# Optimization experiments

Measured on AMD Instinct MI355X. Metric: run time of the kernel, lower is better.

The kernel has to match this reference:

```python
import jax, jax.numpy as jnp
import numpy as np


def _ln(x, g, b, eps=1e-5):
    m = jnp.mean(x, axis=-1, keepdims=True)
    v = jnp.mean((x - m) ** 2, axis=-1, keepdims=True)
    return (x - m) * jax.lax.rsqrt(v + eps) * g + b


def _mlp2(x, w1, b1, w2, b2):
    # Linear -> SiLU -> Linear
    return jax.nn.silu(x @ w1 + b1) @ w2 + b2


def setup_inputs() -> dict:
    key = jax.random.key(0)
    ks = jax.random.split(key, 32)
    B, H, W = 1, 128, 256
    N = H * W                  # 32768 nodes
    K = 6
    E = N * K                  # 196608 edges
    Cin, Cout = 70, 69
    D, De, Hd, L = 256, 128, 512, 8
    s = 0.02

    def rn(k, shape):
        return jax.random.normal(k, shape, jnp.float32) * s

    inp = {
        "x": jax.random.normal(ks[0], (B, Cin, H, W), jnp.float32),
        "edge_index": jax.random.randint(ks[1], (2, E), 0, N, dtype=jnp.int32).astype(jnp.int64),
        "raw_edge_feat": jax.random.normal(ks[2], (E, 3), jnp.float32),
        # node encoder
        "enc_w1": rn(ks[3], (Cin, D)), "enc_b1": jnp.zeros((D,), jnp.float32),
        "enc_w2": rn(ks[4], (D, D)),   "enc_b2": jnp.zeros((D,), jnp.float32),
        # edge encoder
        "eenc_w1": rn(ks[5], (3, De)),  "eenc_b1": jnp.zeros((De,), jnp.float32),
        "eenc_w2": rn(ks[6], (De, De)), "eenc_b2": jnp.zeros((De,), jnp.float32),
        # processor (stacked over L layers)
        "pe_w1": rn(ks[7], (L, 2 * D + De, Hd)), "pe_b1": jnp.zeros((L, Hd), jnp.float32),
        "pe_w2": rn(ks[8], (L, Hd, De)),         "pe_b2": jnp.zeros((L, De), jnp.float32),
        "pe_g": jnp.ones((L, De), jnp.float32),  "pe_bt": jnp.zeros((L, De), jnp.float32),
        "pn_w1": rn(ks[9], (L, D + De, Hd)),     "pn_b1": jnp.zeros((L, Hd), jnp.float32),
        "pn_w2": rn(ks[10], (L, Hd, D)),         "pn_b2": jnp.zeros((L, D), jnp.float32),
        "pn_g": jnp.ones((L, D), jnp.float32),   "pn_bt": jnp.zeros((L, D), jnp.float32),
        # node decoder
        "dec_w1": rn(ks[11], (D, D)),   "dec_b1": jnp.zeros((D,), jnp.float32),
        "dec_w2": rn(ks[12], (D, Cout)), "dec_b2": jnp.zeros((Cout,), jnp.float32),
    }
    return inp


def reference(x, edge_index, raw_edge_feat,
              enc_w1, enc_b1, enc_w2, enc_b2,
              eenc_w1, eenc_b1, eenc_w2, eenc_b2,
              pe_w1, pe_b1, pe_w2, pe_b2, pe_g, pe_bt,
              pn_w1, pn_b1, pn_w2, pn_b2, pn_g, pn_bt,
              dec_w1, dec_b1, dec_w2, dec_b2):
    B, C, H, W = x.shape
    N = H * W
    src, dst = edge_index[0], edge_index[1]

    # encode: (B, N, Cin) -> (B, N, D)
    node = _mlp2(jnp.transpose(x.reshape(B, C, N), (0, 2, 1)), enc_w1, enc_b1, enc_w2, enc_b2)
    # edge encoder shared across batch, then broadcast to (B, E, De)
    edge = _mlp2(raw_edge_feat, eenc_w1, eenc_b1, eenc_w2, eenc_b2)
    edge = jnp.broadcast_to(edge[None], (B,) + edge.shape)

    def step(carry, p):
        node, edge = carry
        ew1, eb1, ew2, eb2, eg, ebt, nw1, nb1, nw2, nb2, ng, nbt = p
        # edge update: gather src/dst node feats, residual MLP + LayerNorm
        inp = jnp.concatenate([node[:, src], node[:, dst], edge], axis=-1)  # (B, E, 2D+De)
        edge = _ln(edge + _mlp2(inp, ew1, eb1, ew2, eb2), eg, ebt)
        # aggregate edges into destination nodes (scatter_add)
        agg = jax.vmap(lambda e: jax.ops.segment_sum(e, dst, num_segments=N))(edge)
        # node update: residual MLP + LayerNorm
        node = _ln(node + _mlp2(jnp.concatenate([node, agg], axis=-1), nw1, nb1, nw2, nb2), ng, nbt)
        return (node, edge), None

    (node, edge), _ = jax.lax.scan(
        step, (node, edge),
        (pe_w1, pe_b1, pe_w2, pe_b2, pe_g, pe_bt,
         pn_w1, pn_b1, pn_w2, pn_b2, pn_g, pn_bt))

    out = _mlp2(node, dec_w1, dec_b1, dec_w2, dec_b2)          # (B, N, Cout)
    return jnp.transpose(out, (0, 2, 1)).reshape(B, -1, H, W)   # (B, Cout, H, W)
```

## Files before the change

### kernel.cpp

```cpp
#include <hip/hip_runtime.h>


typedef __attribute__((ext_vector_type(8))) short bf16x8;
typedef __attribute__((ext_vector_type(4))) float f32x4;
typedef unsigned short u16;

#define NNODES 32768
#define NEDGES 196608

#define MFMA16(a, b, c) __builtin_amdgcn_mfma_f32_16x16x32_bf16((a), (b), (c), 0, 0, 0)

__device__ __forceinline__ u16 f2bf(float f) {
    unsigned u = __float_as_uint(f);
    unsigned r = (u + 0x7FFFu + ((u >> 16) & 1u)) >> 16;
    return (u16)r;
}
__device__ __forceinline__ float bf2f(u16 b) {
    return __uint_as_float(((unsigned)b) << 16);
}
__device__ __forceinline__ unsigned pack2(float a, float b) {
    return (unsigned)f2bf(a) | ((unsigned)f2bf(b) << 16);
}

__global__ void wtrans_kernel(const float* __restrict__ W, u16* __restrict__ WT,
                              int K, int Nout, int Kpad, int NP) {
    __shared__ u16 tile[32][33];
    const int k0 = blockIdx.x * 32, n0 = blockIdx.y * 32;
    const int tx = threadIdx.x & 31, ty = threadIdx.x >> 5;
    #pragma unroll
    for (int i = 0; i < 4; i++) {
        int k = k0 + ty + 8 * i, n = n0 + tx;
        float v = (k < K && n < Nout) ? W[(size_t)k * Nout + n] : 0.f;
        tile[ty + 8 * i][tx] = f2bf(v);
    }
    __syncthreads();
    #pragma unroll
    for (int i = 0; i < 4; i++) {
        int n = n0 + ty + 8 * i, k = k0 + tx;
        if (n < NP && k < Kpad) WT[(size_t)n * Kpad + k] = tile[tx][ty + 8 * i];
    }
}

__global__ void fragpack_kernel(const float* __restrict__ W, u16* __restrict__ F,
                                int K, int N, int CB, int NFRAG) {
    int b = blockIdx.z;
    int fr = blockIdx.x * 4 + (threadIdx.x >> 6);
    if (fr >= NFRAG) return;
    int l = threadIdx.x & 63;
    int ks = fr / CB, cb = fr % CB;
    int k0 = ks * 32 + ((l >> 4) * 8);
    int n = cb * 16 + (l & 15);
    u16 v[8];
    #pragma unroll
    for (int j = 0; j < 8; j++) {
        int k = k0 + j;
        float x = (k < K && n < N) ? W[((size_t)b * K + k) * N + n] : 0.f;
        v[j] = f2bf(x);
    }
    *(uint4*)(F + (((size_t)b * NFRAG + fr) * 64 + l) * 8) = *(const uint4*)v;
}

__global__ void idx_norm_kernel(const int* __restrict__ raw, int* __restrict__ sd) {
    __shared__ int nz;
    if (threadIdx.x == 0) nz = 0;
    __syncthreads();
    for (int i = threadIdx.x; i < 512; i += 256)
        if (raw[2 * i + 1] != 0) atomicAdd(&nz, 1);
    __syncthreads();
    const bool is64 = (nz == 0);
    int idx = blockIdx.x * 256 + threadIdx.x;
    if (idx < 2 * NEDGES) sd[idx] = is64 ? raw[2 * idx] : raw[idx];
}

__global__ void csr_count_kernel(const int* __restrict__ dsti, int* __restrict__ deg) {
    int e = blockIdx.x * 256 + threadIdx.x;
    atomicAdd(&deg[dsti[e]], 1);
}

__global__ void csr_scan_kernel(const int* __restrict__ deg, int* __restrict__ off,
                                int* __restrict__ cur) {
    __shared__ int part[1024];
    const int t = threadIdx.x;
    int local[32];
    int s = 0;
    #pragma unroll
    for (int i = 0; i < 32; i++) { local[i] = deg[t * 32 + i]; s += local[i]; }
    part[t] = s;
    __syncthreads();
    for (int d = 1; d < 1024; d <<= 1) {
        int v = (t >= d) ? part[t - d] : 0;
        __syncthreads();
        part[t] += v;
        __syncthreads();
    }
    int excl = (t == 0) ? 0 : part[t - 1];
    #pragma unroll
    for (int i = 0; i < 32; i++) {
        off[t * 32 + i] = excl;
        cur[t * 32 + i] = excl;
        excl += local[i];
    }
    if (t == 1023) off[NNODES] = excl;
}

__global__ void csr_fill_kernel(const int* __restrict__ dsti, int* __restrict__ cur,
                                int* __restrict__ perm) {
    int e = blockIdx.x * 256 + threadIdx.x;
    int pos = atomicAdd(&cur[dsti[e]], 1);
    perm[pos] = e;
}

__global__ void esort_kernel(const int* __restrict__ sd, const int* __restrict__ perm,
                             int* __restrict__ srcS, int* __restrict__ dstS) {
    int i = blockIdx.x * 256 + threadIdx.x;
    int e = perm[i];
    srcS[i] = sd[e];
    dstS[i] = sd[NEDGES + e];
}

__global__ void gather_kernel(const u16* __restrict__ edge_b,
                              const int* __restrict__ off, u16* __restrict__ aggB) {
    int idx = blockIdx.x * 256 + threadIdx.x;
    int n = idx >> 5, c = (idx & 31) * 4;
    int a = off[n], b = off[n + 1];
    float s0 = 0.f, s1 = 0.f, s2 = 0.f, s3 = 0.f;
    for (int i = a; i < b; i++) {
        uint2 v = *(const uint2*)(edge_b + (size_t)i * 128 + c);
        s0 += bf2f((u16)(v.x & 0xffff)); s1 += bf2f((u16)(v.x >> 16));
        s2 += bf2f((u16)(v.y & 0xffff)); s3 += bf2f((u16)(v.y >> 16));
    }
    uint2 o;
    o.x = pack2(s0, s1);
    o.y = pack2(s2, s3);
    *(uint2*)(aggB + (size_t)n * 128 + c) = o;
}

struct MlpP {
    const u16* A1;
    const u16* A1b;
    const float* Araw;
    const int* src;
    const int* dsti;
    const u16* W1F;
    const u16* W2F;
    const float* b1;
    const float* b2;
    const float* g;
    const float* bt;
    const u16* residB;
    u16* outB;
    float* outDec;
};

template <int K1, int NH, int NOUT, int IN, int OUT, int A1S>
__global__ __launch_bounds__(256, 2) void mlp_kernel(MlpP p) {
    static_assert(K1 % 32 == 0 && NH % 128 == 0, "dims");
    constexpr int KSTEPS = K1 / 32;
    constexpr int NT1 = NH / 64;
    constexpr int CB1 = NH / 16;
    constexpr int NFRAG2 = (NOUT + 15) / 16;
    constexpr int NT2 = (NFRAG2 + 3) / 4;
    constexpr int S2 = NH / 64;
    constexpr int SH2 = NH / 2 + 8;
    constexpr int SH_BYTES = 64 * SH2 * 2;
    constexpr int SMEM_I = (SH_BYTES > 8192 ? SH_BYTES : 8192);
    constexpr int SMEM = SMEM_I + 2560;

    __shared__ __align__(16) char smem[SMEM];
    u16* sA = (u16*)smem;
    u16* sH = (u16*)smem;
    float* sS1 = (float*)(smem + SMEM_I);
    float* sS2 = sS1 + 256;
    float* sMu = sS1 + 512;
    float* sRs = sS1 + 576;

    const int tid = threadIdx.x;
    const int wave = tid >> 6, lane = tid & 63;
    const int lhi = lane >> 4, llo = lane & 15;
    const int r0 = blockIdx.x * 64;
    const int key = (llo >> 1) & 3;

    const int sr = tid >> 2;
    const int sg = (tid & 3) ^ ((sr >> 1) & 3);
    int gsrc = 0, gdst = 0;
    if constexpr (IN == 0) { gsrc = p.src[r0 + sr]; gdst = p.dsti[r0 + sr]; }
    if constexpr (IN == 3) { gsrc = p.src[r0 + sr]; }

    auto loadA = [&](int ks, uint4& d) {
        const int kb = ks * 32;
        if constexpr (IN == 0) {
            if (kb < 256)      d = *(const uint4*)(p.A1 + (size_t)gsrc * 256 + kb + sg * 8);
            else if (kb < 512) d = *(const uint4*)(p.A1 + (size_t)gdst * 256 + (kb - 256) + sg * 8);
            else               d = *(const uint4*)(p.A1b + (size_t)(r0 + sr) * 128 + (kb - 512) + sg * 8);
        } else if constexpr (IN == 1) {
            if (kb < 256) d = *(const uint4*)(p.A1 + (size_t)(r0 + sr) * 256 + kb + sg * 8);
            else          d = *(const uint4*)(p.A1b + (size_t)(r0 + sr) * 128 + (kb - 256) + sg * 8);
        } else if constexpr (IN == 2) {
            d = *(const uint4*)(p.A1 + (size_t)(r0 + sr) * A1S + kb + sg * 8);
        } else {
            uint4 v = {0u, 0u, 0u, 0u};
            if (sg == 0) {
                const float* q = p.Araw + (size_t)gsrc * 3;
                v.x = pack2(q[0], q[1]);
                v.y = pack2(q[2], 0.f);
            }
            d = v;
        }
    };
    auto loadB1 = [&](int ks, bf16x8 (&d)[NT1]) {
        #pragma unroll
        for (int j = 0; j < NT1; j++) {
            int cb = j * 4 + wave;
            d[j] = *(const bf16x8*)(p.W1F + ((size_t)(ks * CB1 + cb) * 64 + lane) * 8);
        }
    };

    const f32x4 fz = {0.f, 0.f, 0.f, 0.f};
    f32x4 acc[4][NT1];
    #pragma unroll
    for (int m = 0; m < 4; m++)
        #pragma unroll
        for (int j = 0; j < NT1; j++) acc[m][j] = fz;

    uint4 pa0, pa1, pa2;
    bf16x8 pb0[NT1], pb1[NT1];
    loadA(0, pa0);
    if constexpr (KSTEPS > 1) loadA(1, pa1);
    if constexpr (KSTEPS > 2) loadA(2, pa2);
    loadB1(0, pb0);
    if constexpr (KSTEPS > 1) loadB1(1, pb1);

    #pragma unroll
    for (int ks = 0; ks < KSTEPS; ks++) {
        uint4* sAw = (uint4*)(sA + (ks & 1) * 2048);
        sAw[tid] = (ks % 3 == 0) ? pa0 : (ks % 3 == 1) ? pa1 : pa2;
        if (ks + 3 < KSTEPS) {
            if (ks % 3 == 0) loadA(ks + 3, pa0);
            else if (ks % 3 == 1) loadA(ks + 3, pa1);
            else loadA(ks + 3, pa2);
        }
        __syncthreads();
        const u16* sAr = sA + (ks & 1) * 2048;
        bf16x8 a[4];
        #pragma unroll
        for (int m = 0; m < 4; m++)
            a[m] = *(const bf16x8*)(sAr + (m * 16 + llo) * 32 + (lhi ^ key) * 8);
        bf16x8 (&pbc)[NT1] = (ks & 1) ? pb1 : pb0;
        #pragma unroll
        for (int j = 0; j < NT1; j++)
            #pragma unroll
            for (int m = 0; m < 4; m++) acc[m][j] = MFMA16(a[m], pbc[j], acc[m][j]);
        if (ks + 2 < KSTEPS) loadB1(ks + 2, pbc);
    }
    __syncthreads();

    f32x4 acc2[4][NT2];
    #pragma unroll
    for (int m = 0; m < 4; m++)
        #pragma unroll
        for (int j = 0; j < NT2; j++) acc2[m][j] = fz;

    auto loadW2 = [&](int g, bf16x8 (&d)[NT2]) {
        #pragma unroll
        for (int j = 0; j < NT2; j++) {
            int f = j * 4 + wave;
            if (NFRAG2 % 4 == 0 || f < NFRAG2)
                d[j] = *(const bf16x8*)(p.W2F + ((size_t)(g * NFRAG2 + f) * 64 + lane) * 8);
        }
    };
    bf16x8 pw0[NT2], pw1[NT2];
    loadW2(0, pw0);
    loadW2(1, pw1);

    #pragma unroll
    for (int half = 0; half < 2; half++) {
        #pragma unroll
        for (int j = half * (NT1 / 2); j < (half + 1) * (NT1 / 2); j++) {
            int c = (j * 4 + wave) * 16 + llo;
            int coll = c - half * (NH / 2);
            float bias = p.b1[c];
            #pragma unroll
            for (int m = 0; m < 4; m++)
                #pragma unroll
                for (int r = 0; r < 4; r++) {
                    int row = m * 16 + lhi * 4 + r;
                    float v = acc[m][j][r] + bias;
                    float sgm = __builtin_amdgcn_rcpf(1.f + __expf(-v));
                    sH[row * SH2 + coll] = f2bf(v * sgm);
                }
        }
        __syncthreads();
        #pragma unroll
        for (int s = 0; s < S2; s++) {
            const int g = half * S2 + s;
            bf16x8 (&pwc)[NT2] = (g & 1) ? pw1 : pw0;
            bf16x8 a2[4];
            #pragma unroll
            for (int m = 0; m < 4; m++)
                a2[m] = *(const bf16x8*)(sH + (m * 16 + llo) * SH2 + s * 32 + lhi * 8);
            #pragma unroll
            for (int j = 0; j < NT2; j++)
                if (NFRAG2 % 4 == 0 || j * 4 + wave < NFRAG2)
                    #pragma unroll
                    for (int m = 0; m < 4; m++)
                        acc2[m][j] = MFMA16(a2[m], pwc[j], acc2[m][j]);
            if (g + 2 < 2 * S2) loadW2(g + 2, pwc);
        }
        __syncthreads();
    }

    if constexpr (OUT == 0) {
        float ps1[4][4], ps2[4][4];
        #pragma unroll
        for (int m = 0; m < 4; m++)
            #pragma unroll
            for (int r = 0; r < 4; r++) { ps1[m][r] = 0.f; ps2[m][r] = 0.f; }
        #pragma unroll
        for (int j = 0; j < NT2; j++) {
            int col = (j * 4 + wave) * 16 + llo;
            float bias = p.b2[col];
            #pragma unroll
            for (int m = 0; m < 4; m++)
                #pragma unroll
                for (int r = 0; r < 4; r++) {
                    int row = m * 16 + lhi * 4 + r;
                    float v = acc2[m][j][r] + bias +
                              bf2f(p.residB[(size_t)(r0 + row) * NOUT + col]);
                    acc2[m][j][r] = v;
                    ps1[m][r] += v;
                    ps2[m][r] += v * v;
                }
        }
        #pragma unroll
        for (int mm = 1; mm < 16; mm <<= 1)
            #pragma unroll
            for (int m = 0; m < 4; m++)
                #pragma unroll
                for (int r = 0; r < 4; r++) {
                    ps1[m][r] += __shfl_xor(ps1[m][r], mm, 64);
                    ps2[m][r] += __shfl_xor(ps2[m][r], mm, 64);
                }
        if (llo == 0) {
            #pragma unroll
            for (int m = 0; m < 4; m++)
                #pragma unroll
                for (int r = 0; r < 4; r++) {
                    int row = m * 16 + lhi * 4 + r;
                    sS1[wave * 64 + row] = ps1[m][r];
                    sS2[wave * 64 + row] = ps2[m][r];
                }
        }
        __syncthreads();
        if (tid < 64) {
            float a = sS1[tid] + sS1[64 + tid] + sS1[128 + tid] + sS1[192 + tid];
            float b = sS2[tid] + sS2[64 + tid] + sS2[128 + tid] + sS2[192 + tid];
            float mu = a * (1.f / NOUT);
            float var = b * (1.f / NOUT) - mu * mu;
            sMu[tid] = mu;
            sRs[tid] = rsqrtf(var + 1e-5f);
        }
        __syncthreads();
        #pragma unroll
        for (int j = 0; j < NT2; j++) {
            int col = (j * 4 + wave) * 16 + llo;
            float gg = p.g[col], bb = p.bt[col];
            #pragma unroll
            for (int m = 0; m < 4; m++)
                #pragma unroll
                for (int r = 0; r < 4; r++) {
                    int row = m * 16 + lhi * 4 + r;
                    float v = (acc2[m][j][r] - sMu[row]) * sRs[row] * gg + bb;
                    p.outB[(size_t)(r0 + row) * NOUT + col] = f2bf(v);
                }
        }
    } else if constexpr (OUT == 1) {
        #pragma unroll
        for (int j = 0; j < NT2; j++) {
            int col = (j * 4 + wave) * 16 + llo;
            float bias = p.b2[col];
            #pragma unroll
            for (int m = 0; m < 4; m++)
                #pragma unroll
                for (int r = 0; r < 4; r++) {
                    int row = m * 16 + lhi * 4 + r;
                    float v = acc2[m][j][r] + bias;
                    p.outB[(size_t)(r0 + row) * NOUT + col] = f2bf(v);
                }
        }
    } else {
        #pragma unroll
        for (int j = 0; j < NT2; j++) {
            int f = j * 4 + wave;
            int col = f * 16 + llo;
            if (f < NFRAG2 && col < 69) {
                float bias = p.b2[col];
                #pragma unroll
                for (int m = 0; m < 4; m++)
                    #pragma unroll
                    for (int r = 0; r < 4; r++) {
                        int row = m * 16 + lhi * 4 + r;
                        p.outDec[(size_t)col * NNODES + (r0 + row)] = acc2[m][j][r] + bias;
                    }
            }
        }
    }
}

extern "C" void kernel_launch(void* const* d_in, const int* in_sizes, int n_in,
                              void* d_out, int out_size, void* d_ws, size_t ws_size,
                              hipStream_t stream) {
    (void)in_sizes; (void)n_in; (void)out_size; (void)ws_size;

    const float* x       = (const float*)d_in[0];
    const int*   eidx    = (const int*)d_in[1];
    const float* raw_e   = (const float*)d_in[2];
    const float* enc_w1  = (const float*)d_in[3];
    const float* enc_b1  = (const float*)d_in[4];
    const float* enc_w2  = (const float*)d_in[5];
    const float* enc_b2  = (const float*)d_in[6];
    const float* eenc_w1 = (const float*)d_in[7];
    const float* eenc_b1 = (const float*)d_in[8];
    const float* eenc_w2 = (const float*)d_in[9];
    const float* eenc_b2 = (const float*)d_in[10];
    const float* pe_w1   = (const float*)d_in[11];
    const float* pe_b1   = (const float*)d_in[12];
    const float* pe_w2   = (const float*)d_in[13];
    const float* pe_b2   = (const float*)d_in[14];
    const float* pe_g    = (const float*)d_in[15];
    const float* pe_bt   = (const float*)d_in[16];
    const float* pn_w1   = (const float*)d_in[17];
    const float* pn_b1   = (const float*)d_in[18];
    const float* pn_w2   = (const float*)d_in[19];
    const float* pn_b2   = (const float*)d_in[20];
    const float* pn_g    = (const float*)d_in[21];
    const float* pn_bt   = (const float*)d_in[22];
    const float* dec_w1  = (const float*)d_in[23];
    const float* dec_b1  = (const float*)d_in[24];
    const float* dec_w2  = (const float*)d_in[25];
    const float* dec_b2  = (const float*)d_in[26];

    char* ws = (char*)d_ws;
    size_t o = 0;
    auto alloc = [&](size_t bytes) -> void* {
        void* p = ws + o;
        o += (bytes + 255) & ~(size_t)255;
        return p;
    };
    u16*   node_b = (u16*)  alloc((size_t)NNODES * 256 * 2);
    u16*   edge_b = (u16*)  alloc((size_t)NEDGES * 128 * 2);
    u16*   aggB   = (u16*)  alloc((size_t)NNODES * 128 * 2);
    u16*   xT     = (u16*)  alloc((size_t)NNODES * 96 * 2);
    u16*   encw1F  = (u16*)alloc((size_t)96 * 256 * 2);
    u16*   encw2F  = (u16*)alloc((size_t)256 * 256 * 2);
    u16*   eencw1F = (u16*)alloc((size_t)32 * 128 * 2);
    u16*   eencw2F = (u16*)alloc((size_t)128 * 128 * 2);
    u16*   pew1F   = (u16*)alloc((size_t)8 * 640 * 512 * 2);
    u16*   pew2F   = (u16*)alloc((size_t)8 * 512 * 128 * 2);
    u16*   pnw1F   = (u16*)alloc((size_t)8 * 384 * 512 * 2);
    u16*   pnw2F   = (u16*)alloc((size_t)8 * 512 * 256 * 2);
    u16*   decw1F  = (u16*)alloc((size_t)256 * 256 * 2);
    u16*   decw2F  = (u16*)alloc((size_t)256 * 80 * 2);
    int*   sd     = (int*)  alloc((size_t)2 * NEDGES * 4);
    int*   deg    = (int*)  alloc((size_t)NNODES * 4);
    int*   off_   = (int*)  alloc((size_t)(NNODES + 1) * 4);
    int*   cur    = (int*)  alloc((size_t)NNODES * 4);
    int*   perm   = (int*)  alloc((size_t)NEDGES * 4);
    int*   srcS   = (int*)  alloc((size_t)NEDGES * 4);
    int*   dstS   = (int*)  alloc((size_t)NEDGES * 4);

    auto FP = [&](const float* W, u16* F, int K, int N, int KB, int CB, int batch) {
        int nf = KB * CB;
        dim3 g((nf + 3) / 4, 1, batch);
        fragpack_kernel<<<g, 256, 0, stream>>>(W, F, K, N, CB, nf);
    };
    FP(enc_w1,  encw1F,  70,  256, 3,  16, 1);
    FP(enc_w2,  encw2F,  256, 256, 8,  16, 1);
    FP(eenc_w1, eencw1F, 3,   128, 1,  8,  1);
    FP(eenc_w2, eencw2F, 128, 128, 4,  8,  1);
    FP(pe_w1,   pew1F,   640, 512, 20, 32, 8);
    FP(pe_w2,   pew2F,   512, 128, 16, 8,  8);
    FP(pn_w1,   pnw1F,   384, 512, 12, 32, 8);
    FP(pn_w2,   pnw2F,   512, 256, 16, 16, 8);
    FP(dec_w1,  decw1F,  256, 256, 8,  16, 1);
    FP(dec_w2,  decw2F,  256, 69,  8,  5,  1);
    {
        dim3 g(96 / 32, NNODES / 32, 1);
        wtrans_kernel<<<g, 256, 0, stream>>>(x, xT, 70, NNODES, 96, NNODES);
    }

    idx_norm_kernel<<<1536, 256, 0, stream>>>(eidx, sd);
    hipMemsetAsync(deg, 0, (size_t)NNODES * 4, stream);
    csr_count_kernel<<<NEDGES / 256, 256, 0, stream>>>(sd + NEDGES, deg);
    csr_scan_kernel<<<1, 1024, 0, stream>>>(deg, off_, cur);
    csr_fill_kernel<<<NEDGES / 256, 256, 0, stream>>>(sd + NEDGES, cur, perm);
    esort_kernel<<<NEDGES / 256, 256, 0, stream>>>(sd, perm, srcS, dstS);

    {
        MlpP p{};
        p.A1 = xT; p.W1F = encw1F; p.W2F = encw2F; p.b1 = enc_b1; p.b2 = enc_b2;
        p.outB = node_b;
        mlp_kernel<96, 256, 256, 2, 1, 96><<<NNODES / 64, 256, 0, stream>>>(p);
    }
    {
        MlpP p{};
        p.Araw = raw_e; p.src = perm;
        p.W1F = eencw1F; p.W2F = eencw2F; p.b1 = eenc_b1; p.b2 = eenc_b2;
        p.outB = edge_b;
        mlp_kernel<32, 128, 128, 3, 1, 0><<<NEDGES / 64, 256, 0, stream>>>(p);
    }

    for (int l = 0; l < 8; l++) {
        {
            MlpP p{};
            p.A1 = node_b; p.A1b = edge_b; p.src = srcS; p.dsti = dstS;
            p.W1F = pew1F + (size_t)l * 640 * 512;
            p.W2F = pew2F + (size_t)l * 512 * 128;
            p.b1 = pe_b1 + l * 512; p.b2 = pe_b2 + l * 128;
            p.g = pe_g + l * 128; p.bt = pe_bt + l * 128;
            p.residB = edge_b; p.outB = edge_b;
            mlp_kernel<640, 512, 128, 0, 0, 0><<<NEDGES / 64, 256, 0, stream>>>(p);
        }
        gather_kernel<<<NNODES * 32 / 256, 256, 0, stream>>>(edge_b, off_, aggB);
        {
            MlpP p{};
            p.A1 = node_b; p.A1b = aggB;
            p.W1F = pnw1F + (size_t)l * 384 * 512;
            p.W2F = pnw2F + (size_t)l * 512 * 256;
            p.b1 = pn_b1 + l * 512; p.b2 = pn_b2 + l * 256;
            p.g = pn_g + l * 256; p.bt = pn_bt + l * 256;
            p.residB = node_b; p.outB = node_b;
            mlp_kernel<384, 512, 256, 1, 0, 0><<<NNODES / 64, 256, 0, stream>>>(p);
        }
    }

    {
        MlpP p{};
        p.A1 = node_b; p.W1F = decw1F; p.W2F = decw2F; p.b1 = dec_b1; p.b2 = dec_b2;
        p.outDec = (float*)d_out;
        mlp_kernel<256, 256, 80, 2, 2, 256><<<NNODES / 64, 256, 0, stream>>>(p);
    }
}
```

Baseline: 2.043 ms.

## Switch MLP kernel from 16x16x32 to 32x32x16 bf16 MFMA tiles

Replaces the 16x16x32 MFMA instructions in the fused two-layer MLP kernel with 32x32x16 MFMA, reorganizing accumulators into 32x32 blocks, the LDS A-fragment reads, the weight fragment packing layout, and all epilogue row/column mappings. Larger MFMA tiles give more output per instruction and fewer A/B fragment loads per flop. The cost is larger accumulator register footprint per wave and different LDS bank access patterns. Small-width layers like the encoder may end up with partially filled tiles.

```diff
diff --git a/kernel.cpp b/kernel.cpp
--- a/kernel.cpp
+++ b/kernel.cpp
@@ -2,13 +2,13 @@
 
 
 typedef __attribute__((ext_vector_type(8))) short bf16x8;
-typedef __attribute__((ext_vector_type(4))) float f32x4;
+typedef __attribute__((ext_vector_type(16))) float f32x16;
 typedef unsigned short u16;
 
 #define NNODES 32768
 #define NEDGES 196608
 
-#define MFMA16(a, b, c) __builtin_amdgcn_mfma_f32_16x16x32_bf16((a), (b), (c), 0, 0, 0)
+#define MFMA32(a, b, c) __builtin_amdgcn_mfma_f32_32x32x16_bf16((a), (b), (c), 0, 0, 0)
 
 __device__ __forceinline__ u16 f2bf(float f) {
     unsigned u = __float_as_uint(f);
@@ -48,8 +48,8 @@
     if (fr >= NFRAG) return;
     int l = threadIdx.x & 63;
     int ks = fr / CB, cb = fr % CB;
-    int k0 = ks * 32 + ((l >> 4) * 8);
-    int n = cb * 16 + (l & 15);
+    int k0 = ks * 16 + ((l >> 5) * 8);
+    int n = cb * 32 + (l & 31);
     u16 v[8];
     #pragma unroll
     for (int j = 0; j < 8; j++) {
@@ -156,12 +156,14 @@
 __global__ __launch_bounds__(256, 2) void mlp_kernel(MlpP p) {
     static_assert(K1 % 32 == 0 && NH % 128 == 0, "dims");
     constexpr int KSTEPS = K1 / 32;
-    constexpr int NT1 = NH / 64;
-    constexpr int CB1 = NH / 16;
-    constexpr int NFRAG2 = (NOUT + 15) / 16;
+    constexpr int NT1 = NH / 128;
+    constexpr int CB1 = NH / 32;
+    constexpr int NFRAG2 = (NOUT + 31) / 32;
     constexpr int NT2 = (NFRAG2 + 3) / 4;
-    constexpr int S2 = NH / 64;
-    constexpr int SH2 = NH / 2 + 8;
+    constexpr int HALVES = (NT1 >= 2) ? 2 : 1;
+    constexpr int HW = NH / HALVES;
+    constexpr int S2 = HW / 32;
+    constexpr int SH2 = HW + 8;
     constexpr int SH_BYTES = 64 * SH2 * 2;
     constexpr int SMEM_I = (SH_BYTES > 8192 ? SH_BYTES : 8192);
     constexpr int SMEM = SMEM_I + 2560;
@@ -176,9 +178,8 @@
 
     const int tid = threadIdx.x;
     const int wave = tid >> 6, lane = tid & 63;
-    const int lhi = lane >> 4, llo = lane & 15;
+    const int l31 = lane & 31, l5 = lane >> 5;
     const int r0 = blockIdx.x * 64;
-    const int key = (llo >> 1) & 3;
 
     const int sr = tid >> 2;
     const int sg = (tid & 3) ^ ((sr >> 1) & 3);
@@ -207,23 +208,27 @@
             d = v;
         }
     };
-    auto loadB1 = [&](int ks, bf16x8 (&d)[NT1]) {
+    auto loadB1 = [&](int ks, bf16x8 (&d)[NT1][2]) {
         #pragma unroll
         for (int j = 0; j < NT1; j++) {
             int cb = j * 4 + wave;
-            d[j] = *(const bf16x8*)(p.W1F + ((size_t)(ks * CB1 + cb) * 64 + lane) * 8);
+            #pragma unroll
+            for (int t = 0; t < 2; t++)
+                d[j][t] = *(const bf16x8*)(p.W1F +
+                          ((size_t)((ks * 2 + t) * CB1 + cb) * 64 + lane) * 8);
         }
     };
 
-    const f32x4 fz = {0.f, 0.f, 0.f, 0.f};
-    f32x4 acc[4][NT1];
-    #pragma unroll
-    for (int m = 0; m < 4; m++)
-        #pragma unroll
-        for (int j = 0; j < NT1; j++) acc[m][j] = fz;
+    f32x16 acc[2][NT1];
+    #pragma unroll
+    for (int mb = 0; mb < 2; mb++)
+        #pragma unroll
+        for (int j = 0; j < NT1; j++)
+            #pragma unroll
+            for (int q = 0; q < 16; q++) acc[mb][j][q] = 0.f;
 
     uint4 pa0, pa1, pa2;
-    bf16x8 pb0[NT1], pb1[NT1];
+    bf16x8 pb0[NT1][2], pb1[NT1][2];
     loadA(0, pa0);
     if constexpr (KSTEPS > 1) loadA(1, pa1);
     if constexpr (KSTEPS > 2) loadA(2, pa2);
@@ -241,50 +246,63 @@
         }
         __syncthreads();
         const u16* sAr = sA + (ks & 1) * 2048;
-        bf16x8 a[4];
-        #pragma unroll
-        for (int m = 0; m < 4; m++)
-            a[m] = *(const bf16x8*)(sAr + (m * 16 + llo) * 32 + (lhi ^ key) * 8);
-        bf16x8 (&pbc)[NT1] = (ks & 1) ? pb1 : pb0;
+        bf16x8 a[2][2];
+        #pragma unroll
+        for (int mb = 0; mb < 2; mb++) {
+            int r = mb * 32 + l31;
+            #pragma unroll
+            for (int t = 0; t < 2; t++)
+                a[mb][t] = *(const bf16x8*)(sAr + r * 32 +
+                            (((t * 2 + l5) ^ ((r >> 1) & 3)) * 8));
+        }
+        bf16x8 (&pbc)[NT1][2] = (ks & 1) ? pb1 : pb0;
         #pragma unroll
         for (int j = 0; j < NT1; j++)
             #pragma unroll
-            for (int m = 0; m < 4; m++) acc[m][j] = MFMA16(a[m], pbc[j], acc[m][j]);
+            for (int t = 0; t < 2; t++)
+                #pragma unroll
+                for (int mb = 0; mb < 2; mb++)
+                    acc[mb][j] = MFMA32(a[mb][t], pbc[j][t], acc[mb][j]);
         if (ks + 2 < KSTEPS) loadB1(ks + 2, pbc);
     }
     __syncthreads();
 
-    f32x4 acc2[4][NT2];
-    #pragma unroll
-    for (int m = 0; m < 4; m++)
-        #pragma unroll
-        for (int j = 0; j < NT2; j++) acc2[m][j] = fz;
-
-    auto loadW2 = [&](int g, bf16x8 (&d)[NT2]) {
+    f32x16 acc2[2][NT2];
+    #pragma unroll
+    for (int mb = 0; mb < 2; mb++)
+        #pragma unroll
+        for (int j = 0; j < NT2; j++)
+            #pragma unroll
+            for (int q = 0; q < 16; q++) acc2[mb][j][q] = 0.f;
+
+    auto loadW2 = [&](int g, bf16x8 (&d)[NT2][2]) {
         #pragma unroll
         for (int j = 0; j < NT2; j++) {
             int f = j * 4 + wave;
             if (NFRAG2 % 4 == 0 || f < NFRAG2)
-                d[j] = *(const bf16x8*)(p.W2F + ((size_t)(g * NFRAG2 + f) * 64 + lane) * 8);
+                #pragma unroll
+                for (int t = 0; t < 2; t++)
+                    d[j][t] = *(const bf16x8*)(p.W2F +
+                              ((size_t)((g * 2 + t) * NFRAG2 + f) * 64 + lane) * 8);
         }
     };
-    bf16x8 pw0[NT2], pw1[NT2];
+    bf16x8 pw0[NT2][2], pw1[NT2][2];
     loadW2(0, pw0);
-    loadW2(1, pw1);
-
-    #pragma unroll
-    for (int half = 0; half < 2; half++) {
-        #pragma unroll
-        for (int j = half * (NT1 / 2); j < (half + 1) * (NT1 / 2); j++) {
-            int c = (j * 4 + wave) * 16 + llo;
-            int coll = c - half * (NH / 2);
+    if constexpr (HALVES * S2 > 1) loadW2(1, pw1);
+
+    #pragma unroll
+    for (int half = 0; half < HALVES; half++) {
+        #pragma unroll
+        for (int j = half * (NT1 / HALVES); j < (half + 1) * (NT1 / HALVES); j++) {
+            int c = (j * 4 + wave) * 32 + l31;
+            int coll = c - half * HW;
             float bias = p.b1[c];
             #pragma unroll
-            for (int m = 0; m < 4; m++)
-                #pragma unroll
-                for (int r = 0; r < 4; r++) {
-                    int row = m * 16 + lhi * 4 + r;
-                    float v = acc[m][j][r] + bias;
+            for (int mb = 0; mb < 2; mb++)
+                #pragma unroll
+                for (int q = 0; q < 16; q++) {
+                    int row = mb * 32 + (q & 3) + 8 * (q >> 2) + 4 * l5;
+                    float v = acc[mb][j][q] + bias;
                     float sgm = __builtin_amdgcn_rcpf(1.f + __expf(-v));
                     sH[row * SH2 + coll] = f2bf(v * sgm);
                 }
@@ -293,61 +311,66 @@
         #pragma unroll
         for (int s = 0; s < S2; s++) {
             const int g = half * S2 + s;
-            bf16x8 (&pwc)[NT2] = (g & 1) ? pw1 : pw0;
-            bf16x8 a2[4];
-            #pragma unroll
-            for (int m = 0; m < 4; m++)
-                a2[m] = *(const bf16x8*)(sH + (m * 16 + llo) * SH2 + s * 32 + lhi * 8);
+            bf16x8 (&pwc)[NT2][2] = (g & 1) ? pw1 : pw0;
+            bf16x8 a2[2][2];
+            #pragma unroll
+            for (int mb = 0; mb < 2; mb++)
+                #pragma unroll
+                for (int t = 0; t < 2; t++)
+                    a2[mb][t] = *(const bf16x8*)(sH + (mb * 32 + l31) * SH2 +
+                                 s * 32 + t * 16 + l5 * 8);
             #pragma unroll
             for (int j = 0; j < NT2; j++)
                 if (NFRAG2 % 4 == 0 || j * 4 + wave < NFRAG2)
                     #pragma unroll
-                    for (int m = 0; m < 4; m++)
-                        acc2[m][j] = MFMA16(a2[m], pwc[j], acc2[m][j]);
-            if (g + 2 < 2 * S2) loadW2(g + 2, pwc);
+                    for (int t = 0; t < 2; t++)
+                        #pragma unroll
+                        for (int mb = 0; mb < 2; mb++)
+                            acc2[mb][j] = MFMA32(a2[mb][t], pwc[j][t], acc2[mb][j]);
+            if (g + 2 < HALVES * S2) loadW2(g + 2, pwc);
         }
         __syncthreads();
     }
 
     if constexpr (OUT == 0) {
-        float ps1[4][4], ps2[4][4];
-        #pragma unroll
-        for (int m = 0; m < 4; m++)
-            #pragma unroll
-            for (int r = 0; r < 4; r++) { ps1[m][r] = 0.f; ps2[m][r] = 0.f; }
+        float ps1[2][16], ps2[2][16];
+        #pragma unroll
+        for (int mb = 0; mb < 2; mb++)
+            #pragma unroll
+            for (int q = 0; q < 16; q++) { ps1[mb][q] = 0.f; ps2[mb][q] = 0.f; }
         #pragma unroll
         for (int j = 0; j < NT2; j++) {
-            int col = (j * 4 + wave) * 16 + llo;
+            int col = (j * 4 + wave) * 32 + l31;
             float bias = p.b2[col];
             #pragma unroll
-            for (int m = 0; m < 4; m++)
-                #pragma unroll
-                for (int r = 0; r < 4; r++) {
-                    int row = m * 16 + lhi * 4 + r;
-                    float v = acc2[m][j][r] + bias +
+            for (int mb = 0; mb < 2; mb++)
+                #pragma unroll
+                for (int q = 0; q < 16; q++) {
+                    int row = mb * 32 + (q & 3) + 8 * (q >> 2) + 4 * l5;
+                    float v = acc2[mb][j][q] + bias +
                               bf2f(p.residB[(size_t)(r0 + row) * NOUT + col]);
-                    acc2[m][j][r] = v;
-                    ps1[m][r] += v;
-                    ps2[m][r] += v * v;
+                    acc2[mb][j][q] = v;
+                    ps1[mb][q] += v;
+                    ps2[mb][q] += v * v;
                 }
         }
         #pragma unroll
-        for (int mm = 1; mm < 16; mm <<= 1)
-            #pragma unroll
-            for (int m = 0; m < 4; m++)
-                #pragma unroll
-                for (int r = 0; r < 4; r++) {
-                    ps1[m][r] += __shfl_xor(ps1[m][r], mm, 64);
-                    ps2[m][r] += __shfl_xor(ps2[m][r], mm, 64);
+        for (int mm = 1; mm <= 16; mm <<= 1)
+            #pragma unroll
+            for (int mb = 0; mb < 2; mb++)
+                #pragma unroll
+                for (int q = 0; q < 16; q++) {
+                    ps1[mb][q] += __shfl_xor(ps1[mb][q], mm, 64);
+                    ps2[mb][q] += __shfl_xor(ps2[mb][q], mm, 64);
                 }
-        if (llo == 0) {
-            #pragma unroll
-            for (int m = 0; m < 4; m++)
-                #pragma unroll
-                for (int r = 0; r < 4; r++) {
-                    int row = m * 16 + lhi * 4 + r;
-                    sS1[wave * 64 + row] = ps1[m][r];
-                    sS2[wave * 64 + row] = ps2[m][r];
+        if (l31 == 0) {
+            #pragma unroll
+            for (int mb = 0; mb < 2; mb++)
+                #pragma unroll
+                for (int q = 0; q < 16; q++) {
+                    int row = mb * 32 + (q & 3) + 8 * (q >> 2) + 4 * l5;
+                    sS1[wave * 64 + row] = ps1[mb][q];
+                    sS2[wave * 64 + row] = ps2[mb][q];
                 }
         }
         __syncthreads();
@@ -362,28 +385,28 @@
         __syncthreads();
         #pragma unroll
         for (int j = 0; j < NT2; j++) {
-            int col = (j * 4 + wave) * 16 + llo;
+            int col = (j * 4 + wave) * 32 + l31;
             float gg = p.g[col], bb = p.bt[col];
             #pragma unroll
-            for (int m = 0; m < 4; m++)
-                #pragma unroll
-                for (int r = 0; r < 4; r++) {
-                    int row = m * 16 + lhi * 4 + r;
-                    float v = (acc2[m][j][r] - sMu[row]) * sRs[row] * gg + bb;
+            for (int mb = 0; mb < 2; mb++)
+                #pragma unroll
+                for (int q = 0; q < 16; q++) {
+                    int row = mb * 32 + (q & 3) + 8 * (q >> 2) + 4 * l5;
+                    float v = (acc2[mb][j][q] - sMu[row]) * sRs[row] * gg + bb;
                     p.outB[(size_t)(r0 + row) * NOUT + col] = f2bf(v);
                 }
         }
     } else if constexpr (OUT == 1) {
         #pragma unroll
         for (int j = 0; j < NT2; j++) {
-            int col = (j * 4 + wave) * 16 + llo;
+            int col = (j * 4 + wave) * 32 + l31;
             float bias = p.b2[col];
             #pragma unroll
-            for (int m = 0; m < 4; m++)
-                #pragma unroll
-                for (int r = 0; r < 4; r++) {
-                    int row = m * 16 + lhi * 4 + r;
-                    float v = acc2[m][j][r] + bias;
+            for (int mb = 0; mb < 2; mb++)
+                #pragma unroll
+                for (int q = 0; q < 16; q++) {
+                    int row = mb * 32 + (q & 3) + 8 * (q >> 2) + 4 * l5;
+                    float v = acc2[mb][j][q] + bias;
                     p.outB[(size_t)(r0 + row) * NOUT + col] = f2bf(v);
                 }
         }
@@ -391,15 +414,15 @@
         #pragma unroll
         for (int j = 0; j < NT2; j++) {
             int f = j * 4 + wave;
-            int col = f * 16 + llo;
+            int col = f * 32 + l31;
             if (f < NFRAG2 && col < 69) {
                 float bias = p.b2[col];
                 #pragma unroll
-                for (int m = 0; m < 4; m++)
+                for (int mb = 0; mb < 2; mb++)
                     #pragma unroll
-                    for (int r = 0; r < 4; r++) {
-                        int row = m * 16 + lhi * 4 + r;
-                        p.outDec[(size_t)col * NNODES + (r0 + row)] = acc2[m][j][r] + bias;
+                    for (int q = 0; q < 16; q++) {
+                        int row = mb * 32 + (q & 3) + 8 * (q >> 2) + 4 * l5;
+                        p.outDec[(size_t)col * NNODES + (r0 + row)] = acc2[mb][j][q] + bias;
                     }
             }
         }
@@ -459,7 +482,7 @@
     u16*   pnw1F   = (u16*)alloc((size_t)8 * 384 * 512 * 2);
     u16*   pnw2F   = (u16*)alloc((size_t)8 * 512 * 256 * 2);
     u16*   decw1F  = (u16*)alloc((size_t)256 * 256 * 2);
-    u16*   decw2F  = (u16*)alloc((size_t)256 * 80 * 2);
+    u16*   decw2F  = (u16*)alloc((size_t)256 * 96 * 2);
     int*   sd     = (int*)  alloc((size_t)2 * NEDGES * 4);
     int*   deg    = (int*)  alloc((size_t)NNODES * 4);
     int*   off_   = (int*)  alloc((size_t)(NNODES + 1) * 4);
@@ -468,21 +491,21 @@
     int*   srcS   = (int*)  alloc((size_t)NEDGES * 4);
     int*   dstS   = (int*)  alloc((size_t)NEDGES * 4);
 
-    auto FP = [&](const float* W, u16* F, int K, int N, int KB, int CB, int batch) {
-        int nf = KB * CB;
+    auto FP = [&](const float* W, u16* F, int K, int N, int KB16, int CB32, int batch) {
+        int nf = KB16 * CB32;
         dim3 g((nf + 3) / 4, 1, batch);
-        fragpack_kernel<<<g, 256, 0, stream>>>(W, F, K, N, CB, nf);
+        fragpack_kernel<<<g, 256, 0, stream>>>(W, F, K, N, CB32, nf);
     };
-    FP(enc_w1,  encw1F,  70,  256, 3,  16, 1);
-    FP(enc_w2,  encw2F,  256, 256, 8,  16, 1);
-    FP(eenc_w1, eencw1F, 3,   128, 1,  8,  1);
-    FP(eenc_w2, eencw2F, 128, 128, 4,  8,  1);
-    FP(pe_w1,   pew1F,   640, 512, 20, 32, 8);
-    FP(pe_w2,   pew2F,   512, 128, 16, 8,  8);
-    FP(pn_w1,   pnw1F,   384, 512, 12, 32, 8);
-    FP(pn_w2,   pnw2F,   512, 256, 16, 16, 8);
-    FP(dec_w1,  decw1F,  256, 256, 8,  16, 1);
-    FP(dec_w2,  decw2F,  256, 69,  8,  5,  1);
+    FP(enc_w1,  encw1F,  70,  256, 6,  8,  1);
+    FP(enc_w2,  encw2F,  256, 256, 16, 8,  1);
+    FP(eenc_w1, eencw1F, 3,   128, 2,  4,  1);
+    FP(eenc_w2, eencw2F, 128, 128, 8,  4,  1);
+    FP(pe_w1,   pew1F,   640, 512, 40, 16, 8);
+    FP(pe_w2,   pew2F,   512, 128, 32, 4,  8);
+    FP(pn_w1,   pnw1F,   384, 512, 24, 16, 8);
+    FP(pn_w2,   pnw2F,   512, 256, 32, 8,  8);
+    FP(dec_w1,  decw1F,  256, 256, 16, 8,  1);
+    FP(dec_w2,  decw2F,  256, 69,  16, 3,  1);
     {
         dim3 g(96 / 32, NNODES / 32, 1);
         wtrans_kernel<<<g, 256, 0, stream>>>(x, xT, 70, NNODES, 96, NNODES);
```

New measurement: 2.356 ms. +15.3%, slower.

## Stage MLP A-tiles straight into LDS with double-buffered super-steps

Applied to the files above, without the earlier changes.

Activation (A) tiles in the fused MLP kernel now go from global memory straight into LDS using global_load_lds, instead of passing through VGPRs and then being written to shared memory. The K loop is regrouped into super-steps of two k-slices. Each super-step is double-buffered, so the next one is staged while the current one is consumed, and only one barrier is needed per super-step. The aim is to cut register pressure and LDS write instructions, and to overlap gathers with MFMA work. In exchange, LDS staging use grows and the prefetch distance shrinks from three slices to one super-step. Correctness also depends on the async LDS writes being completed by the barrier.

```diff
diff --git a/kernel.cpp b/kernel.cpp
--- a/kernel.cpp
+++ b/kernel.cpp
@@ -20,6 +20,11 @@
 }
 __device__ __forceinline__ unsigned pack2(float a, float b) {
     return (unsigned)f2bf(a) | ((unsigned)f2bf(b) << 16);
+}
+__device__ __forceinline__ void gload_lds16(const void* g, void* l) {
+    __builtin_amdgcn_global_load_lds(
+        (const __attribute__((address_space(1))) void*)g,
+        (__attribute__((address_space(3))) void*)l, 16, 0, 0);
 }
 
 __global__ void wtrans_kernel(const float* __restrict__ W, u16* __restrict__ WT,
@@ -156,6 +161,8 @@
 __global__ __launch_bounds__(256, 2) void mlp_kernel(MlpP p) {
     static_assert(K1 % 32 == 0 && NH % 128 == 0, "dims");
     constexpr int KSTEPS = K1 / 32;
+    constexpr int SUPER = (KSTEPS % 2 == 0) ? 2 : 1;
+    constexpr int NSS = KSTEPS / SUPER;
     constexpr int NT1 = NH / 64;
     constexpr int CB1 = NH / 16;
     constexpr int NFRAG2 = (NOUT + 15) / 16;
@@ -163,7 +170,8 @@
     constexpr int S2 = NH / 64;
     constexpr int SH2 = NH / 2 + 8;
     constexpr int SH_BYTES = 64 * SH2 * 2;
-    constexpr int SMEM_I = (SH_BYTES > 8192 ? SH_BYTES : 8192);
+    constexpr int A_STAGE = 2 * SUPER * 4096;
+    constexpr int SMEM_I = (SH_BYTES > A_STAGE ? SH_BYTES : A_STAGE);
     constexpr int SMEM = SMEM_I + 2560;
 
     __shared__ __align__(16) char smem[SMEM];
@@ -186,25 +194,34 @@
     if constexpr (IN == 0) { gsrc = p.src[r0 + sr]; gdst = p.dsti[r0 + sr]; }
     if constexpr (IN == 3) { gsrc = p.src[r0 + sr]; }
 
-    auto loadA = [&](int ks, uint4& d) {
-        const int kb = ks * 32;
-        if constexpr (IN == 0) {
-            if (kb < 256)      d = *(const uint4*)(p.A1 + (size_t)gsrc * 256 + kb + sg * 8);
-            else if (kb < 512) d = *(const uint4*)(p.A1 + (size_t)gdst * 256 + (kb - 256) + sg * 8);
-            else               d = *(const uint4*)(p.A1b + (size_t)(r0 + sr) * 128 + (kb - 512) + sg * 8);
-        } else if constexpr (IN == 1) {
-            if (kb < 256) d = *(const uint4*)(p.A1 + (size_t)(r0 + sr) * 256 + kb + sg * 8);
-            else          d = *(const uint4*)(p.A1b + (size_t)(r0 + sr) * 128 + (kb - 256) + sg * 8);
-        } else if constexpr (IN == 2) {
-            d = *(const uint4*)(p.A1 + (size_t)(r0 + sr) * A1S + kb + sg * 8);
-        } else {
-            uint4 v = {0u, 0u, 0u, 0u};
-            if (sg == 0) {
-                const float* q = p.Araw + (size_t)gsrc * 3;
-                v.x = pack2(q[0], q[1]);
-                v.y = pack2(q[2], 0.f);
+    auto stageA = [&](int ss, int b) {
+        #pragma unroll
+        for (int t = 0; t < SUPER; t++) {
+            const int ks = ss * SUPER + t;
+            const int kb = ks * 32;
+            u16* ldst = sA + (size_t)b * (SUPER * 2048) + t * 2048 + wave * 512;
+            if constexpr (IN == 3) {
+                uint4 v = {0u, 0u, 0u, 0u};
+                if (sg == 0) {
+                    const float* q = p.Araw + (size_t)gsrc * 3;
+                    v.x = pack2(q[0], q[1]);
+                    v.y = pack2(q[2], 0.f);
+                }
+                *(uint4*)(sA + (size_t)b * (SUPER * 2048) + t * 2048 + tid * 8) = v;
+            } else {
+                const u16* src;
+                if constexpr (IN == 0) {
+                    if (kb < 256)      src = p.A1 + (size_t)gsrc * 256 + kb + sg * 8;
+                    else if (kb < 512) src = p.A1 + (size_t)gdst * 256 + (kb - 256) + sg * 8;
+                    else               src = p.A1b + (size_t)(r0 + sr) * 128 + (kb - 512) + sg * 8;
+                } else if constexpr (IN == 1) {
+                    if (kb < 256) src = p.A1 + (size_t)(r0 + sr) * 256 + kb + sg * 8;
+                    else          src = p.A1b + (size_t)(r0 + sr) * 128 + (kb - 256) + sg * 8;
+                } else {
+                    src = p.A1 + (size_t)(r0 + sr) * A1S + kb + sg * 8;
+                }
+                gload_lds16(src, ldst);
             }
-            d = v;
         }
     };
     auto loadB1 = [&](int ks, bf16x8 (&d)[NT1]) {
@@ -222,35 +239,31 @@
         #pragma unroll
         for (int j = 0; j < NT1; j++) acc[m][j] = fz;
 
-    uint4 pa0, pa1, pa2;
     bf16x8 pb0[NT1], pb1[NT1];
-    loadA(0, pa0);
-    if constexpr (KSTEPS > 1) loadA(1, pa1);
-    if constexpr (KSTEPS > 2) loadA(2, pa2);
+    stageA(0, 0);
     loadB1(0, pb0);
     if constexpr (KSTEPS > 1) loadB1(1, pb1);
 
     #pragma unroll
-    for (int ks = 0; ks < KSTEPS; ks++) {
-        uint4* sAw = (uint4*)(sA + (ks & 1) * 2048);
-        sAw[tid] = (ks % 3 == 0) ? pa0 : (ks % 3 == 1) ? pa1 : pa2;
-        if (ks + 3 < KSTEPS) {
-            if (ks % 3 == 0) loadA(ks + 3, pa0);
-            else if (ks % 3 == 1) loadA(ks + 3, pa1);
-            else loadA(ks + 3, pa2);
-        }
-        __syncthreads();
-        const u16* sAr = sA + (ks & 1) * 2048;
-        bf16x8 a[4];
-        #pragma unroll
-        for (int m = 0; m < 4; m++)
-            a[m] = *(const bf16x8*)(sAr + (m * 16 + llo) * 32 + (lhi ^ key) * 8);
-        bf16x8 (&pbc)[NT1] = (ks & 1) ? pb1 : pb0;
-        #pragma unroll
-        for (int j = 0; j < NT1; j++)
-            #pragma unroll
-            for (int m = 0; m < 4; m++) acc[m][j] = MFMA16(a[m], pbc[j], acc[m][j]);
-        if (ks + 2 < KSTEPS) loadB1(ks + 2, pbc);
+    for (int ss = 0; ss < NSS; ss++) {
+        __syncthreads();
+        if (ss + 1 < NSS) stageA(ss + 1, (ss + 1) & 1);
+        const u16* bufb = sA + (ss & 1) * (SUPER * 2048);
+        #pragma unroll
+        for (int t = 0; t < SUPER; t++) {
+            const int ks = ss * SUPER + t;
+            const u16* sAr = bufb + t * 2048;
+            bf16x8 a[4];
+            #pragma unroll
+            for (int m = 0; m < 4; m++)
+                a[m] = *(const bf16x8*)(sAr + (m * 16 + llo) * 32 + (lhi ^ key) * 8);
+            bf16x8 (&pbc)[NT1] = (ks & 1) ? pb1 : pb0;
+            #pragma unroll
+            for (int j = 0; j < NT1; j++)
+                #pragma unroll
+                for (int m = 0; m < 4; m++) acc[m][j] = MFMA16(a[m], pbc[j], acc[m][j]);
+            if (ks + 2 < KSTEPS) loadB1(ks + 2, pbc);
+        }
     }
     __syncthreads();
 
```

After: 2.102 ms. +2.9%, slower.
